# Kernel optimization log

Measured on AMD Instinct MI355X. Metric: run time of the kernel, lower is better.

## Reference

```python
import jax, jax.numpy as jnp
import numpy as np

B, S, D = 2, 2048, 2048
H, HD = 16, 128  # n_heads, head_dim = dim // n_heads
NEG_INF = -1e9


def setup_inputs() -> dict:
    key = jax.random.key(0)
    ks = jax.random.split(key, 6)
    x = jax.random.normal(ks[0], (B, S, D), dtype=jnp.float32)
    # freqs_complex as (real, imag) pairs; unused downstream because the
    # source's apply_rotary_emb returns its input unchanged (x.type_as(x)).
    freqs_complex = jax.random.normal(ks[1], (S, HD // 2, 2), dtype=jnp.float32)
    # causal additive mask [1, 1, S, S]
    causal = jnp.tril(jnp.ones((S, S), dtype=bool))
    mask = jnp.where(causal, 0.0, NEG_INF).astype(jnp.float32)[None, None]
    wq = jax.random.normal(ks[2], (D, D), dtype=jnp.float32) * 0.02
    wk = jax.random.normal(ks[3], (D, D), dtype=jnp.float32) * 0.02
    wv = jax.random.normal(ks[4], (D, D), dtype=jnp.float32) * 0.02
    wo = jax.random.normal(ks[5], (D, D), dtype=jnp.float32) * 0.02
    return {"x": x, "freqs_complex": freqs_complex, "mask": mask,
            "wq": wq, "wk": wk, "wv": wv, "wo": wo}


def reference(x, freqs_complex, mask, wq, wk, wv, wo):
    b, s, d = x.shape
    # QKV projections (torch Linear: x @ W.T), reshape to [B, S, H, HD]
    q = (x @ wq.T).reshape(b, s, H, HD)
    k = (x @ wk.T).reshape(b, s, H, HD)
    v = (x @ wv.T).reshape(b, s, H, HD)
    # apply_rotary_emb in the source returns its input unchanged -> no-op.
    scale = 1.0 / jnp.sqrt(jnp.asarray(HD, dtype=x.dtype))
    scores = jnp.einsum('bshd,bthd->bhst', q, k) * scale + mask
    probs = jax.nn.softmax(scores.astype(jnp.float32), axis=-1).astype(q.dtype)
    out = jnp.einsum('bhst,bthd->bshd', probs, v).reshape(b, s, H * HD)
    return out @ wo.T
```

## Files before the change

kernel.cpp:

```cpp
#include <hip/hip_runtime.h>
#include <hip/hip_bf16.h>
#include <stdint.h>


namespace {

constexpr int kB = 2;
constexpr int kS = 2048;
constexpr int kD = 2048;
constexpr int kH = 16;
constexpr int kHD = 128;
constexpr int kM = kB * kS;

typedef __attribute__((ext_vector_type(8))) __bf16 bf16x8;
typedef __attribute__((ext_vector_type(4))) float f32x4;

__device__ __forceinline__ unsigned short f2bf(float x) {
  uint32_t u = __float_as_uint(x);
  u += 0x7fffu + ((u >> 16) & 1u);
  return (unsigned short)(u >> 16);
}

__device__ __forceinline__ void gld_lds16(const void* g, void* l) {
  __builtin_amdgcn_global_load_lds((__attribute__((address_space(1))) void*)g,
                                   (__attribute__((address_space(3))) void*)l,
                                   16, 0, 0);
}

__global__ void cvt_all(const float* __restrict__ x, const float* __restrict__ wq,
                        const float* __restrict__ wk, const float* __restrict__ wv,
                        const float* __restrict__ wo, unsigned short* __restrict__ xb,
                        unsigned short* __restrict__ wqkv) {
  constexpr int n4 = kD * kD / 4;
  const int i = blockIdx.x * blockDim.x + threadIdx.x;
  const int y = blockIdx.y;
  const float* src;
  unsigned short* dst;
  float s = 1.0f;
  if (y < 2) {
    src = x + (size_t)y * n4 * 4;
    dst = xb + (size_t)y * n4 * 4;
  } else {
    src = (y == 2) ? wq : (y == 3) ? wk : (y == 4) ? wv : wo;
    dst = wqkv + (size_t)(y - 2) * n4 * 4;
    if (y == 2) s = 0.08838834764831845f * 1.44269504088896340736f;
  }
  float4 v = ((const float4*)src)[i];
  ushort4 o;
  o.x = f2bf(v.x * s); o.y = f2bf(v.y * s); o.z = f2bf(v.z * s); o.w = f2bf(v.w * s);
  ((ushort4*)dst)[i] = o;
}

template <bool OUT_BF16>
__global__ __launch_bounds__(256, 2) void gemm_bt(
    const unsigned short* __restrict__ A, const unsigned short* __restrict__ W,
    void* __restrict__ C, int M, int N, int K) {
  __shared__ unsigned short Asm[128 * 64];
  __shared__ unsigned short Bsm[128 * 64];
  const int t = threadIdx.x;
  const int wave = t >> 6, lane = t & 63;
  const int ln = lane & 15, quad = lane >> 4;
  const int wr = wave >> 1, wc = wave & 1;
  const int m0 = blockIdx.y * 128, n0 = blockIdx.x * 128;

  const int srow = t >> 3;
  const int scol = ((t & 7) ^ (srow & 7)) << 3;
  const unsigned short* gA = A + (size_t)(m0 + srow) * K + scol;
  const unsigned short* gW = W + (size_t)(n0 + srow) * K + scol;
  const size_t g32 = (size_t)32 * K;
  unsigned short* lA = Asm + wave * 512;
  unsigned short* lB = Bsm + wave * 512;

  f32x4 acc[4][4] = {};

  for (int k0 = 0; k0 < K; k0 += 64) {
    __syncthreads();
#pragma unroll
    for (int i = 0; i < 4; ++i) {
      gld_lds16(gA + i * g32, lA + i * 2048);
      gld_lds16(gW + i * g32, lB + i * 2048);
    }
    gA += 64; gW += 64;
    __syncthreads();

#pragma unroll
    for (int kk = 0; kk < 2; ++kk) {
      bf16x8 af[4], bw[4];
#pragma unroll
      for (int mt = 0; mt < 4; ++mt) {
        const int row = wr * 64 + mt * 16 + ln;
        af[mt] = *(const bf16x8*)(Asm + row * 64 +
                                  (((kk * 4 + quad) ^ (row & 7)) << 3));
      }
#pragma unroll
      for (int nt = 0; nt < 4; ++nt) {
        const int row = wc * 64 + nt * 16 + ln;
        bw[nt] = *(const bf16x8*)(Bsm + row * 64 +
                                  (((kk * 4 + quad) ^ (row & 7)) << 3));
      }
#pragma unroll
      for (int mt = 0; mt < 4; ++mt)
#pragma unroll
        for (int nt = 0; nt < 4; ++nt)
          acc[mt][nt] = __builtin_amdgcn_mfma_f32_16x16x32_bf16(
              af[mt], bw[nt], acc[mt][nt], 0, 0, 0);
    }
  }

  const int cm = m0 + wr * 64 + quad * 4;
  const int cn = n0 + wc * 64 + ln;
#pragma unroll
  for (int mt = 0; mt < 4; ++mt)
#pragma unroll
    for (int r = 0; r < 4; ++r) {
      const size_t rowoff = (size_t)(cm + mt * 16 + r) * N + cn;
      if (OUT_BF16) {
        unsigned short* Cb = (unsigned short*)C;
#pragma unroll
        for (int nt = 0; nt < 4; ++nt) Cb[rowoff + nt * 16] = f2bf(acc[mt][nt][r]);
      } else {
        float* Cf = (float*)C;
#pragma unroll
        for (int nt = 0; nt < 4; ++nt) Cf[rowoff + nt * 16] = acc[mt][nt][r];
      }
    }
}

__global__ __launch_bounds__(256, 2) void gemm_qkv(
    const unsigned short* __restrict__ A, const unsigned short* __restrict__ W,
    unsigned short* __restrict__ Qb, unsigned short* __restrict__ Kb,
    unsigned short* __restrict__ Vt) {
  constexpr int K = 2048;
  __shared__ unsigned short Asm[128 * 64];
  __shared__ unsigned short Bsm[128 * 64];
  const int t = threadIdx.x;
  const int wave = t >> 6, lane = t & 63;
  const int ln = lane & 15, quad = lane >> 4;
  const int wr = wave >> 1, wc = wave & 1;
  const int m0 = blockIdx.y * 128, n0 = blockIdx.x * 128;

  const int srow = t >> 3;
  const int scol = ((t & 7) ^ (srow & 7)) << 3;
  const unsigned short* gA = A + (size_t)(m0 + srow) * K + scol;
  const unsigned short* gW = W + (size_t)(n0 + srow) * K + scol;
  const size_t g32 = (size_t)32 * K;
  unsigned short* lA = Asm + wave * 512;
  unsigned short* lB = Bsm + wave * 512;

  f32x4 acc[4][4] = {};

  for (int k0 = 0; k0 < K; k0 += 64) {
    __syncthreads();
#pragma unroll
    for (int i = 0; i < 4; ++i) {
      gld_lds16(gA + i * g32, lA + i * 2048);
      gld_lds16(gW + i * g32, lB + i * 2048);
    }
    gA += 64; gW += 64;
    __syncthreads();

#pragma unroll
    for (int kk = 0; kk < 2; ++kk) {
      bf16x8 af[4], bw[4];
#pragma unroll
      for (int mt = 0; mt < 4; ++mt) {
        const int row = wr * 64 + mt * 16 + ln;
        af[mt] = *(const bf16x8*)(Asm + row * 64 +
                                  (((kk * 4 + quad) ^ (row & 7)) << 3));
      }
#pragma unroll
      for (int nt = 0; nt < 4; ++nt) {
        const int row = wc * 64 + nt * 16 + ln;
        bw[nt] = *(const bf16x8*)(Bsm + row * 64 +
                                  (((kk * 4 + quad) ^ (row & 7)) << 3));
      }
#pragma unroll
      for (int mt = 0; mt < 4; ++mt)
#pragma unroll
        for (int nt = 0; nt < 4; ++nt)
          acc[mt][nt] = __builtin_amdgcn_mfma_f32_16x16x32_bf16(
              af[mt], bw[nt], acc[mt][nt], 0, 0, 0);
    }
  }

  const int cm = m0 + wr * 64 + quad * 4;
  const int cn = n0 + wc * 64 + ln;
  if (n0 < 4096) {
    unsigned short* dst = (n0 < 2048) ? Qb : Kb;
    const int cnl = cn & 2047;
#pragma unroll
    for (int mt = 0; mt < 4; ++mt)
#pragma unroll
      for (int r = 0; r < 4; ++r) {
        const size_t rowoff = (size_t)(cm + mt * 16 + r) * kD + cnl;
#pragma unroll
        for (int nt = 0; nt < 4; ++nt) dst[rowoff + nt * 16] = f2bf(acc[mt][nt][r]);
      }
  } else {
#pragma unroll
    for (int mt = 0; mt < 4; ++mt)
#pragma unroll
      for (int r = 0; r < 4; ++r) {
        const int m = cm + mt * 16 + r;
        const int bb = m >> 11, s = m & 2047;
#pragma unroll
        for (int nt = 0; nt < 4; ++nt) {
          const int d = cn + nt * 16 - 4096;
          Vt[((size_t)(bb * 2048 + d)) * (size_t)kS + s] = f2bf(acc[mt][nt][r]);
        }
      }
  }
}

__global__ __launch_bounds__(256, 3) void flash_attn(
    const unsigned short* __restrict__ Q, const unsigned short* __restrict__ Kb,
    const unsigned short* __restrict__ Vt, unsigned short* __restrict__ Ob) {
  __shared__ unsigned short Ksm[64 * 128];
  __shared__ unsigned short Vsm[128 * 64];
  __shared__ unsigned short Psm[4][2048];
  const int t = threadIdx.x;
  const int wave = t >> 6, lane = t & 63;
  const int ln = lane & 15, quad = lane >> 4;
  const int bx = blockIdx.x;
  const int gq = bx >> 5;
  const int qt = (gq < 8) ? (15 - gq) : (gq - 8);
  const int bh = bx & 31, b = bh >> 4, h = bh & 15;
  const int q0 = qt * 128;

  bf16x8 qf[2][4];
#pragma unroll
  for (int st = 0; st < 2; ++st) {
    const size_t qoff =
        ((size_t)(b * kS + q0 + st * 64 + wave * 16 + ln)) * kD + h * kHD;
#pragma unroll
    for (int ks = 0; ks < 4; ++ks)
      qf[st][ks] = *(const bf16x8*)(Q + qoff + ks * 32 + quad * 8);
  }

  float lsum[2] = {0.0f, 0.0f};
  f32x4 oa[2][8] = {};

  const int krow = t >> 4;
  const unsigned short* gK =
      Kb + ((size_t)(b * kS) + krow) * kD + h * kHD + (((t & 15) ^ krow) << 3);
  const int vrow = t >> 3;
  const unsigned short* gV =
      Vt + ((size_t)(bh * 128 + vrow)) * kS + (((t & 7) ^ (vrow & 7)) << 3);

  const int nIter = 2 * qt + 2;

  for (int it = 0; it < nIter; ++it) {
    const int kv0 = it << 6;
    __syncthreads();
#pragma unroll
    for (int i = 0; i < 4; ++i)
      gld_lds16(gK + ((size_t)kv0 + i * 16) * kD, Ksm + i * 2048 + wave * 512);
#pragma unroll
    for (int i = 0; i < 4; ++i)
      gld_lds16(gV + (size_t)i * 32 * kS + kv0, Vsm + i * 2048 + wave * 512);
    __syncthreads();

    f32x4 sc[2][4] = {};
#pragma unroll
    for (int ct = 0; ct < 4; ++ct) {
      const int row = ct * 16 + ln;
#pragma unroll
      for (int ks = 0; ks < 4; ++ks) {
        bf16x8 kf =
            *(const bf16x8*)(Ksm + row * 128 + (((ks * 4 + quad) ^ ln) << 3));
#pragma unroll
        for (int st = 0; st < 2; ++st)
          sc[st][ct] = __builtin_amdgcn_mfma_f32_16x16x32_bf16(
              kf, qf[st][ks], sc[st][ct], 0, 0, 0);
      }
    }

#pragma unroll
    for (int st = 0; st < 2; ++st) {
      const int q_lo = q0 + st * 64 + wave * 16;
      const bool full = (kv0 + 63 <= q_lo);
      const int qs = q_lo + ln;
      float ls = 0.0f;
#pragma unroll
      for (int ct = 0; ct < 4; ++ct) {
        const int kvb = kv0 + ct * 16 + quad * 4;
        float p[4];
#pragma unroll
        for (int r = 0; r < 4; ++r) {
          float s = sc[st][ct][r];
          if (!full && (kvb + r > qs)) s = -1e30f;
          p[r] = exp2f(s);
          ls += p[r];
        }
        const uint32_t u0 = (uint32_t)f2bf(p[0]) | ((uint32_t)f2bf(p[1]) << 16);
        const uint32_t u1 = (uint32_t)f2bf(p[2]) | ((uint32_t)f2bf(p[3]) << 16);
        const int cs = (ct * 4 + quad) ^ (ln & 14);
        uint2 u; u.x = u0; u.y = u1;
        *(uint2*)(&Psm[wave][(st * 16 + ln) * 64 + cs * 4]) = u;
      }
      lsum[st] += ls;
    }

    bf16x8 pf[2][2];
#pragma unroll
    for (int st = 0; st < 2; ++st)
#pragma unroll
      for (int ks = 0; ks < 2; ++ks)
        pf[st][ks] = *(const bf16x8*)(
            &Psm[wave][(st * 16 + ln) * 64 +
                       (((ks * 8 + quad * 2) ^ (ln & 14)) << 2)]);
#pragma unroll
    for (int ct = 0; ct < 8; ++ct) {
      const int row = ct * 16 + ln;
#pragma unroll
      for (int ks = 0; ks < 2; ++ks) {
        bf16x8 vf =
            *(const bf16x8*)(Vsm + row * 64 + (((ks * 4 + quad) ^ (ln & 7)) << 3));
#pragma unroll
        for (int st = 0; st < 2; ++st)
          oa[st][ct] = __builtin_amdgcn_mfma_f32_16x16x32_bf16(
              pf[st][ks], vf, oa[st][ct], 0, 0, 0);
      }
    }
  }

#pragma unroll
  for (int st = 0; st < 2; ++st) {
    float l = lsum[st];
    l += __shfl_xor(l, 16, 64);
    l += __shfl_xor(l, 32, 64);
    float inv[4];
#pragma unroll
    for (int r = 0; r < 4; ++r)
      inv[r] = 1.0f / __shfl(l, (lane & 48) | (quad * 4 + r), 64);
#pragma unroll
    for (int r = 0; r < 4; ++r) {
      const size_t orow =
          ((size_t)(b * kS + q0 + st * 64 + wave * 16 + quad * 4 + r)) * kD +
          h * kHD + ln;
#pragma unroll
      for (int ct = 0; ct < 8; ++ct) Ob[orow + ct * 16] = f2bf(oa[st][ct][r] * inv[r]);
    }
  }
}

}

extern "C" void kernel_launch(void* const* d_in, const int* in_sizes, int n_in,
                              void* d_out, int out_size, void* d_ws, size_t ws_size,
                              hipStream_t stream) {
  (void)in_sizes; (void)n_in; (void)out_size; (void)ws_size;
  const float* x  = (const float*)d_in[0];
  const float* wq = (const float*)d_in[3];
  const float* wk = (const float*)d_in[4];
  const float* wv = (const float*)d_in[5];
  const float* wo = (const float*)d_in[6];
  float* out = (float*)d_out;

  unsigned short* ws   = (unsigned short*)d_ws;
  unsigned short* xb   = ws;
  unsigned short* wqkv = xb + (size_t)kM * kD;
  unsigned short* wob  = wqkv + 3 * (size_t)kD * kD;
  unsigned short* Qb   = wob + (size_t)kD * kD;
  unsigned short* Kbuf = Qb  + (size_t)kM * kD;
  unsigned short* Vt   = Kbuf + (size_t)kM * kD;
  unsigned short* Ab   = Vt + (size_t)kM * kD;

  const int n4 = kD * kD / 4;
  cvt_all<<<dim3(n4 / 256, 6), 256, 0, stream>>>(x, wq, wk, wv, wo, xb, wqkv);

  gemm_qkv<<<dim3(6144 / 128, kM / 128), 256, 0, stream>>>(xb, wqkv, Qb, Kbuf, Vt);

  flash_attn<<<dim3(512), 256, 0, stream>>>(Qb, Kbuf, Vt, Ab);

  gemm_bt<false><<<dim3(kD / 128, kM / 128), 256, 0, stream>>>(Ab, wob, out, kM, kD, kD);
}
```

Measured before the change: 393.5 us.

## Rewrite QKV GEMM with 8-wave 128x384 tiles and double-buffered LDS pipeline

Replaces the 128x128 single-buffered QKV projection GEMM with a 512-thread kernel that computes 128x384 output tiles. It uses double-buffered LDS stages split into 32-wide K halves, issues the next stage's global-to-LDS loads before each MFMA phase, and synchronises with vmcnt waits and raw barriers. It also raises MFMA priority during compute and remaps workgroup ids for locality. The goal is to overlap memory loads with matrix math and raise arithmetic intensity, at the cost of more LDS and register pressure and a mixed per-element output path.

```diff
diff --git a/kernel.cpp b/kernel.cpp
--- a/kernel.cpp
+++ b/kernel.cpp
@@ -51,6 +51,113 @@
   ((ushort4*)dst)[i] = o;
 }
 
+
+#define QKV_STAGE(T2, Q2)                                                      \
+  {                                                                            \
+    const int kof = (T2) * 64 + (Q2) * 32;                                     \
+    const int sbuf = (T2) & 1;                                                 \
+    gld_lds16(gA + kof, &Asm[sbuf][Q2][0] + wave * 512);                       \
+    unsigned short* lb = &Bsm[sbuf][Q2][0] + wave * 512;                       \
+    const unsigned short* gw = gW + kof;                                       \
+    gld_lds16(gw, lb);                                                         \
+    gld_lds16(gw + (size_t)128 * 2048, lb + 4096);                             \
+    gld_lds16(gw + (size_t)256 * 2048, lb + 8192);                             \
+  }
+
+#define QKV_SYNC(VMS)                                                          \
+  asm volatile("s_waitcnt vmcnt(" VMS ")" ::: "memory");                       \
+  __builtin_amdgcn_s_barrier();                                                \
+  asm volatile("" ::: "memory");
+
+#define QKV_PHASE(BUF, Q, DOSTAGE, T2, Q2)                                     \
+  {                                                                            \
+    bf16x8 af[4], bw[6];                                                       \
+    _Pragma("unroll") for (int mt = 0; mt < 4; ++mt) {                         \
+      const int row = wr * 64 + mt * 16 + ln;                                  \
+      af[mt] = *(const bf16x8*)&Asm[BUF][Q][row * 32 +                         \
+                                            ((quad ^ ((row >> 1) & 3)) << 3)]; \
+    }                                                                          \
+    _Pragma("unroll") for (int nt = 0; nt < 6; ++nt) {                         \
+      const int row = wc * 96 + nt * 16 + ln;                                  \
+      bw[nt] = *(const bf16x8*)&Bsm[BUF][Q][row * 32 +                         \
+                                            ((quad ^ ((row >> 1) & 3)) << 3)]; \
+    }                                                                          \
+    if (DOSTAGE) QKV_STAGE(T2, Q2);                                            \
+    __builtin_amdgcn_s_setprio(1);                                             \
+    _Pragma("unroll") for (int mt = 0; mt < 4; ++mt)                           \
+      _Pragma("unroll") for (int nt = 0; nt < 6; ++nt)                         \
+        acc[mt][nt] = __builtin_amdgcn_mfma_f32_16x16x32_bf16(                 \
+            af[mt], bw[nt], acc[mt][nt], 0, 0, 0);                             \
+    __builtin_amdgcn_s_setprio(0);                                             \
+  }
+
+__global__ __launch_bounds__(512, 2) void gemm_qkv8(
+    const unsigned short* __restrict__ A, const unsigned short* __restrict__ W,
+    unsigned short* __restrict__ Qb, unsigned short* __restrict__ Kb,
+    unsigned short* __restrict__ Vt) {
+  constexpr int K = 2048;
+  __shared__ unsigned short Asm[2][2][128 * 32];
+  __shared__ unsigned short Bsm[2][2][384 * 32];
+
+  const int t = threadIdx.x;
+  const int wave = t >> 6, lane = t & 63;
+  const int ln = lane & 15, quad = lane >> 4;
+  const int wr = wave >> 2, wc = wave & 3;
+
+  const int bid = blockIdx.x;
+  const int wg = (bid & 7) * 64 + (bid >> 3);
+  const int n0 = (wg & 15) * 384;
+  const int m0 = (wg >> 4) * 128;
+
+  const int srow = t >> 2;
+  const int scol = ((t & 3) ^ ((t >> 3) & 3)) << 3;
+  const unsigned short* gA = A + (size_t)(m0 + srow) * K + scol;
+  const unsigned short* gW = W + (size_t)(n0 + srow) * K + scol;
+
+  f32x4 acc[4][6] = {};
+
+  QKV_STAGE(0, 0);
+  QKV_STAGE(0, 1);
+  QKV_STAGE(1, 0);
+  QKV_SYNC("8");
+
+  for (int tt = 0; tt < 30; tt += 2) {
+    QKV_PHASE(0, 0, true, tt + 1, 1) QKV_SYNC("8");
+    QKV_PHASE(0, 1, true, tt + 2, 0) QKV_SYNC("8");
+    QKV_PHASE(1, 0, true, tt + 2, 1) QKV_SYNC("8");
+    QKV_PHASE(1, 1, true, tt + 3, 0) QKV_SYNC("8");
+  }
+  QKV_PHASE(0, 0, true, 31, 1) QKV_SYNC("8");
+  QKV_PHASE(0, 1, false, 0, 0) QKV_SYNC("4");
+  QKV_PHASE(1, 0, false, 0, 0) QKV_SYNC("0");
+  QKV_PHASE(1, 1, false, 0, 0)
+
+  const int cm0 = m0 + wr * 64 + quad * 4;
+  const int cn0 = n0 + wc * 96 + ln;
+#pragma unroll
+  for (int mt = 0; mt < 4; ++mt)
+#pragma unroll
+    for (int r = 0; r < 4; ++r) {
+      const int m = cm0 + mt * 16 + r;
+      const int bb = m >> 11, s = m & 2047;
+#pragma unroll
+      for (int nt = 0; nt < 6; ++nt) {
+        const int n = cn0 + nt * 16;
+        const unsigned short v = f2bf(acc[mt][nt][r]);
+        if (n < 2048)
+          Qb[(size_t)m * 2048 + n] = v;
+        else if (n < 4096)
+          Kb[(size_t)m * 2048 + (n - 2048)] = v;
+        else
+          Vt[((size_t)(bb * 2048 + (n - 4096))) * (size_t)kS + s] = v;
+      }
+    }
+}
+
+#undef QKV_PHASE
+#undef QKV_SYNC
+#undef QKV_STAGE
+
 template <bool OUT_BF16>
 __global__ __launch_bounds__(256, 2) void gemm_bt(
     const unsigned short* __restrict__ A, const unsigned short* __restrict__ W,
@@ -124,92 +231,6 @@
         for (int nt = 0; nt < 4; ++nt) Cf[rowoff + nt * 16] = acc[mt][nt][r];
       }
     }
-}
-
-__global__ __launch_bounds__(256, 2) void gemm_qkv(
-    const unsigned short* __restrict__ A, const unsigned short* __restrict__ W,
-    unsigned short* __restrict__ Qb, unsigned short* __restrict__ Kb,
-    unsigned short* __restrict__ Vt) {
-  constexpr int K = 2048;
-  __shared__ unsigned short Asm[128 * 64];
-  __shared__ unsigned short Bsm[128 * 64];
-  const int t = threadIdx.x;
-  const int wave = t >> 6, lane = t & 63;
-  const int ln = lane & 15, quad = lane >> 4;
-  const int wr = wave >> 1, wc = wave & 1;
-  const int m0 = blockIdx.y * 128, n0 = blockIdx.x * 128;
-
-  const int srow = t >> 3;
-  const int scol = ((t & 7) ^ (srow & 7)) << 3;
-  const unsigned short* gA = A + (size_t)(m0 + srow) * K + scol;
-  const unsigned short* gW = W + (size_t)(n0 + srow) * K + scol;
-  const size_t g32 = (size_t)32 * K;
-  unsigned short* lA = Asm + wave * 512;
-  unsigned short* lB = Bsm + wave * 512;
-
-  f32x4 acc[4][4] = {};
-
-  for (int k0 = 0; k0 < K; k0 += 64) {
-    __syncthreads();
-#pragma unroll
-    for (int i = 0; i < 4; ++i) {
-      gld_lds16(gA + i * g32, lA + i * 2048);
-      gld_lds16(gW + i * g32, lB + i * 2048);
-    }
-    gA += 64; gW += 64;
-    __syncthreads();
-
-#pragma unroll
-    for (int kk = 0; kk < 2; ++kk) {
-      bf16x8 af[4], bw[4];
-#pragma unroll
-      for (int mt = 0; mt < 4; ++mt) {
-        const int row = wr * 64 + mt * 16 + ln;
-        af[mt] = *(const bf16x8*)(Asm + row * 64 +
-                                  (((kk * 4 + quad) ^ (row & 7)) << 3));
-      }
-#pragma unroll
-      for (int nt = 0; nt < 4; ++nt) {
-        const int row = wc * 64 + nt * 16 + ln;
-        bw[nt] = *(const bf16x8*)(Bsm + row * 64 +
-                                  (((kk * 4 + quad) ^ (row & 7)) << 3));
-      }
-#pragma unroll
-      for (int mt = 0; mt < 4; ++mt)
-#pragma unroll
-        for (int nt = 0; nt < 4; ++nt)
-          acc[mt][nt] = __builtin_amdgcn_mfma_f32_16x16x32_bf16(
-              af[mt], bw[nt], acc[mt][nt], 0, 0, 0);
-    }
-  }
-
-  const int cm = m0 + wr * 64 + quad * 4;
-  const int cn = n0 + wc * 64 + ln;
-  if (n0 < 4096) {
-    unsigned short* dst = (n0 < 2048) ? Qb : Kb;
-    const int cnl = cn & 2047;
-#pragma unroll
-    for (int mt = 0; mt < 4; ++mt)
-#pragma unroll
-      for (int r = 0; r < 4; ++r) {
-        const size_t rowoff = (size_t)(cm + mt * 16 + r) * kD + cnl;
-#pragma unroll
-        for (int nt = 0; nt < 4; ++nt) dst[rowoff + nt * 16] = f2bf(acc[mt][nt][r]);
-      }
-  } else {
-#pragma unroll
-    for (int mt = 0; mt < 4; ++mt)
-#pragma unroll
-      for (int r = 0; r < 4; ++r) {
-        const int m = cm + mt * 16 + r;
-        const int bb = m >> 11, s = m & 2047;
-#pragma unroll
-        for (int nt = 0; nt < 4; ++nt) {
-          const int d = cn + nt * 16 - 4096;
-          Vt[((size_t)(bb * 2048 + d)) * (size_t)kS + s] = f2bf(acc[mt][nt][r]);
-        }
-      }
-  }
 }
 
 __global__ __launch_bounds__(256, 3) void flash_attn(
@@ -369,7 +390,7 @@
   const int n4 = kD * kD / 4;
   cvt_all<<<dim3(n4 / 256, 6), 256, 0, stream>>>(x, wq, wk, wv, wo, xb, wqkv);
 
-  gemm_qkv<<<dim3(6144 / 128, kM / 128), 256, 0, stream>>>(xb, wqkv, Qb, Kbuf, Vt);
+  gemm_qkv8<<<dim3(512), 512, 0, stream>>>(xb, wqkv, Qb, Kbuf, Vt);
 
   flash_attn<<<dim3(512), 256, 0, stream>>>(Qb, Kbuf, Vt, Ab);
 
```

Result: slower. 421.8 us (+7.2%).

## Rewrite QKV GEMM as 8-wave 256x128 tile with 4-stage LDS pipeline

Applied to the files above, without the earlier changes.

Replaces the QKV projection GEMM with a 512-thread kernel that computes a 256x128 output tile per block. K is split into 32-wide stages held in a 4-deep LDS ring buffer, with global-to-LDS loads issued three stages ahead and synchronised using explicit vmcnt waits and barriers. MFMA sections are raised to high priority with s_setprio. The aim is to hide global load latency and improve operand reuse, at the cost of larger LDS use (96 KB per block) and a hand-scheduled pipeline that is fragile to get right.

```diff
diff --git a/kernel.cpp b/kernel.cpp
--- a/kernel.cpp
+++ b/kernel.cpp
@@ -51,6 +51,133 @@
   ((ushort4*)dst)[i] = o;
 }
 
+#define QKV_STAGE(U)                                                           \
+  {                                                                            \
+    const int u_ = (U);                                                        \
+    const int kof_ = (u_ >> 1) * 64 + (u_ & 1) * 32;                           \
+    unsigned short* const lr_ = &Lds[u_ & 3][0];                               \
+    gld_lds16(gA + kof_, lr_ + wave * 512);                                    \
+    gld_lds16(gA + kof_ + (size_t)128 * 2048, lr_ + 4096 + wave * 512);        \
+    gld_lds16(gW + kof_, lr_ + 8192 + wave * 512);                             \
+  }
+
+#define QKV_SYNC(VMS)                                                          \
+  asm volatile("s_waitcnt vmcnt(" VMS ")" ::: "memory");                       \
+  __builtin_amdgcn_s_barrier();                                                \
+  asm volatile("" ::: "memory");
+
+#define QKV_PHASE(P, DOSTAGE, VMS)                                             \
+  {                                                                            \
+    const int p_ = (P);                                                        \
+    const unsigned short* const Ar = &Lds[p_ & 3][0];                          \
+    const unsigned short* const Br = Ar + 8192;                                \
+    bf16x8 af[4], bw[4];                                                       \
+    _Pragma("unroll") for (int mt = 0; mt < 4; ++mt) {                         \
+      const int row = wr * 64 + mt * 16 + ln;                                  \
+      af[mt] = *(const bf16x8*)(Ar + row * 32 +                                \
+                                ((quad ^ ((row >> 1) & 3)) << 3));             \
+    }                                                                          \
+    _Pragma("unroll") for (int nt = 0; nt < 4; ++nt) {                         \
+      const int row = wc * 64 + nt * 16 + ln;                                  \
+      bw[nt] = *(const bf16x8*)(Br + row * 32 +                                \
+                                ((quad ^ ((row >> 1) & 3)) << 3));             \
+    }                                                                          \
+    if (DOSTAGE) QKV_STAGE(p_ + 3);                                            \
+    __builtin_amdgcn_s_barrier();                                              \
+    __builtin_amdgcn_s_setprio(1);                                             \
+    _Pragma("unroll") for (int mt = 0; mt < 4; ++mt)                           \
+      _Pragma("unroll") for (int nt = 0; nt < 4; ++nt)                         \
+        acc[mt][nt] = __builtin_amdgcn_mfma_f32_16x16x32_bf16(                 \
+            af[mt], bw[nt], acc[mt][nt], 0, 0, 0);                             \
+    __builtin_amdgcn_s_setprio(0);                                             \
+    QKV_SYNC(VMS)                                                              \
+  }
+
+__global__ __launch_bounds__(512, 2) void gemm_qkv8b(
+    const unsigned short* __restrict__ A, const unsigned short* __restrict__ W,
+    unsigned short* __restrict__ Qb, unsigned short* __restrict__ Kb,
+    unsigned short* __restrict__ Vt) {
+  constexpr int K = 2048;
+  __shared__ unsigned short Lds[4][12288];
+
+  const int t = threadIdx.x;
+  const int wave = t >> 6, lane = t & 63;
+  const int ln = lane & 15, quad = lane >> 4;
+  const int wr = wave >> 1, wc = wave & 1;
+
+  const int n0 = blockIdx.x * 128;
+  const int m0 = blockIdx.y * 256;
+
+  const int srow = t >> 2;
+  const int scol = ((t & 3) ^ ((t >> 3) & 3)) << 3;
+  const unsigned short* gA = A + (size_t)(m0 + srow) * K + scol;
+  const unsigned short* gW = W + (size_t)(n0 + srow) * K + scol;
+
+  f32x4 acc[4][4] = {};
+
+  QKV_STAGE(0);
+  QKV_STAGE(1);
+  QKV_STAGE(2);
+  QKV_SYNC("6");
+
+  for (int p = 0; p < 61; ++p) QKV_PHASE(p, true, "6");
+  QKV_PHASE(61, false, "3");
+  QKV_PHASE(62, false, "0");
+  {
+    const unsigned short* const Ar = &Lds[3][0];
+    const unsigned short* const Br = Ar + 8192;
+    bf16x8 af[4], bw[4];
+#pragma unroll
+    for (int mt = 0; mt < 4; ++mt) {
+      const int row = wr * 64 + mt * 16 + ln;
+      af[mt] = *(const bf16x8*)(Ar + row * 32 + ((quad ^ ((row >> 1) & 3)) << 3));
+    }
+#pragma unroll
+    for (int nt = 0; nt < 4; ++nt) {
+      const int row = wc * 64 + nt * 16 + ln;
+      bw[nt] = *(const bf16x8*)(Br + row * 32 + ((quad ^ ((row >> 1) & 3)) << 3));
+    }
+#pragma unroll
+    for (int mt = 0; mt < 4; ++mt)
+#pragma unroll
+      for (int nt = 0; nt < 4; ++nt)
+        acc[mt][nt] = __builtin_amdgcn_mfma_f32_16x16x32_bf16(
+            af[mt], bw[nt], acc[mt][nt], 0, 0, 0);
+  }
+
+  const int cm0 = m0 + wr * 64 + quad * 4;
+  const int cn0 = n0 + wc * 64 + ln;
+  if (n0 < 4096) {
+    unsigned short* dst = (n0 < 2048) ? Qb : Kb;
+    const int nbase = cn0 & 2047;
+#pragma unroll
+    for (int mt = 0; mt < 4; ++mt)
+#pragma unroll
+      for (int r = 0; r < 4; ++r) {
+        const size_t rowoff = (size_t)(cm0 + mt * 16 + r) * kD + nbase;
+#pragma unroll
+        for (int nt = 0; nt < 4; ++nt) dst[rowoff + nt * 16] = f2bf(acc[mt][nt][r]);
+      }
+  } else {
+#pragma unroll
+    for (int mt = 0; mt < 4; ++mt)
+#pragma unroll
+      for (int r = 0; r < 4; ++r) {
+        const int m = cm0 + mt * 16 + r;
+        const int bb = m >> 11, s = m & 2047;
+#pragma unroll
+        for (int nt = 0; nt < 4; ++nt) {
+          const int d = cn0 + nt * 16 - 4096;
+          Vt[((size_t)(bb * 2048 + d)) * (size_t)kS + s] = f2bf(acc[mt][nt][r]);
+        }
+      }
+  }
+}
+
+#undef QKV_PHASE
+#undef QKV_SYNC
+#undef QKV_STAGE
+
 template <bool OUT_BF16>
 __global__ __launch_bounds__(256, 2) void gemm_bt(
     const unsigned short* __restrict__ A, const unsigned short* __restrict__ W,
@@ -124,92 +251,6 @@
         for (int nt = 0; nt < 4; ++nt) Cf[rowoff + nt * 16] = acc[mt][nt][r];
       }
     }
-}
-
-__global__ __launch_bounds__(256, 2) void gemm_qkv(
-    const unsigned short* __restrict__ A, const unsigned short* __restrict__ W,
-    unsigned short* __restrict__ Qb, unsigned short* __restrict__ Kb,
-    unsigned short* __restrict__ Vt) {
-  constexpr int K = 2048;
-  __shared__ unsigned short Asm[128 * 64];
-  __shared__ unsigned short Bsm[128 * 64];
-  const int t = threadIdx.x;
-  const int wave = t >> 6, lane = t & 63;
-  const int ln = lane & 15, quad = lane >> 4;
-  const int wr = wave >> 1, wc = wave & 1;
-  const int m0 = blockIdx.y * 128, n0 = blockIdx.x * 128;
-
-  const int srow = t >> 3;
-  const int scol = ((t & 7) ^ (srow & 7)) << 3;
-  const unsigned short* gA = A + (size_t)(m0 + srow) * K + scol;
-  const unsigned short* gW = W + (size_t)(n0 + srow) * K + scol;
-  const size_t g32 = (size_t)32 * K;
-  unsigned short* lA = Asm + wave * 512;
-  unsigned short* lB = Bsm + wave * 512;
-
-  f32x4 acc[4][4] = {};
-
-  for (int k0 = 0; k0 < K; k0 += 64) {
-    __syncthreads();
-#pragma unroll
-    for (int i = 0; i < 4; ++i) {
-      gld_lds16(gA + i * g32, lA + i * 2048);
-      gld_lds16(gW + i * g32, lB + i * 2048);
-    }
-    gA += 64; gW += 64;
-    __syncthreads();
-
-#pragma unroll
-    for (int kk = 0; kk < 2; ++kk) {
-      bf16x8 af[4], bw[4];
-#pragma unroll
-      for (int mt = 0; mt < 4; ++mt) {
-        const int row = wr * 64 + mt * 16 + ln;
-        af[mt] = *(const bf16x8*)(Asm + row * 64 +
-                                  (((kk * 4 + quad) ^ (row & 7)) << 3));
-      }
-#pragma unroll
-      for (int nt = 0; nt < 4; ++nt) {
-        const int row = wc * 64 + nt * 16 + ln;
-        bw[nt] = *(const bf16x8*)(Bsm + row * 64 +
-                                  (((kk * 4 + quad) ^ (row & 7)) << 3));
-      }
-#pragma unroll
-      for (int mt = 0; mt < 4; ++mt)
-#pragma unroll
-        for (int nt = 0; nt < 4; ++nt)
-          acc[mt][nt] = __builtin_amdgcn_mfma_f32_16x16x32_bf16(
-              af[mt], bw[nt], acc[mt][nt], 0, 0, 0);
-    }
-  }
-
-  const int cm = m0 + wr * 64 + quad * 4;
-  const int cn = n0 + wc * 64 + ln;
-  if (n0 < 4096) {
-    unsigned short* dst = (n0 < 2048) ? Qb : Kb;
-    const int cnl = cn & 2047;
-#pragma unroll
-    for (int mt = 0; mt < 4; ++mt)
-#pragma unroll
-      for (int r = 0; r < 4; ++r) {
-        const size_t rowoff = (size_t)(cm + mt * 16 + r) * kD + cnl;
-#pragma unroll
-        for (int nt = 0; nt < 4; ++nt) dst[rowoff + nt * 16] = f2bf(acc[mt][nt][r]);
-      }
-  } else {
-#pragma unroll
-    for (int mt = 0; mt < 4; ++mt)
-#pragma unroll
-      for (int r = 0; r < 4; ++r) {
-        const int m = cm + mt * 16 + r;
-        const int bb = m >> 11, s = m & 2047;
-#pragma unroll
-        for (int nt = 0; nt < 4; ++nt) {
-          const int d = cn + nt * 16 - 4096;
-          Vt[((size_t)(bb * 2048 + d)) * (size_t)kS + s] = f2bf(acc[mt][nt][r]);
-        }
-      }
-  }
 }
 
 __global__ __launch_bounds__(256, 3) void flash_attn(
@@ -369,7 +410,7 @@
   const int n4 = kD * kD / 4;
   cvt_all<<<dim3(n4 / 256, 6), 256, 0, stream>>>(x, wq, wk, wv, wo, xb, wqkv);
 
-  gemm_qkv<<<dim3(6144 / 128, kM / 128), 256, 0, stream>>>(xb, wqkv, Qb, Kbuf, Vt);
+  gemm_qkv8b<<<dim3(48, 16), 512, 0, stream>>>(xb, wqkv, Qb, Kbuf, Vt);
 
   flash_attn<<<dim3(512), 256, 0, stream>>>(Qb, Kbuf, Vt, Ab);
 
```

Result: no change. 392.4 us (-0.3%).
